# Performance work log

Hardware: AMD Instinct MI355X
Metric: run time of the kernel (lower is better)

The kernel has to match this reference:

```python
import jax, jax.numpy as jnp
import numpy as np

DIM = 1024
N_HEADS = 16
HEAD_DIM = DIM // N_HEADS
MAX_SEQ = 2048
BATCH = 4
SEQ = 2048


def _rope_tables(seq_len, head_dim):
    inv_freq = 1.0 / (10000.0 ** (jnp.arange(0, head_dim, 2, dtype=jnp.float32) / head_dim))
    t = jnp.arange(seq_len, dtype=jnp.float32)
    freqs = jnp.outer(t, inv_freq)            # [S, D/2]
    emb = jnp.concatenate([freqs, freqs], axis=-1)  # [S, D]
    return jnp.cos(emb), jnp.sin(emb)


def setup_inputs() -> dict:
    key = jax.random.key(0)
    kx, kq, kk, kv, ko = jax.random.split(key, 5)
    s = 1.0 / np.sqrt(DIM)
    x = jax.random.normal(kx, (BATCH, SEQ, DIM), dtype=jnp.float32)
    Wq = jax.random.normal(kq, (DIM, DIM), dtype=jnp.float32) * s
    Wk = jax.random.normal(kk, (DIM, DIM), dtype=jnp.float32) * s
    Wv = jax.random.normal(kv, (DIM, DIM), dtype=jnp.float32) * s
    Wo = jax.random.normal(ko, (DIM, DIM), dtype=jnp.float32) * s
    cos, sin = _rope_tables(SEQ, HEAD_DIM)
    mask = jnp.tril(jnp.ones((SEQ, SEQ), dtype=bool))[None, None]  # [1,1,S,S] causal
    return {"x": x, "Wq": Wq, "Wk": Wk, "Wv": Wv, "Wo": Wo,
            "cos": cos, "sin": sin, "mask": mask}


def _rotate_half(t):
    t1, t2 = jnp.split(t, 2, axis=-1)
    return jnp.concatenate([-t2, t1], axis=-1)


def reference(x, Wq, Wk, Wv, Wo, cos, sin, mask):
    B, S, _ = x.shape
    # projections (torch Linear: y = x @ W.T)
    q = (x @ Wq.T).reshape(B, S, N_HEADS, HEAD_DIM)
    k = (x @ Wk.T).reshape(B, S, N_HEADS, HEAD_DIM)
    v = (x @ Wv.T).reshape(B, S, N_HEADS, HEAD_DIM)
    # RoPE on [B,S,H,D]: cos/sin broadcast over batch and heads
    c = cos[None, :S, None, :]
    s_ = sin[None, :S, None, :]
    q = q * c + _rotate_half(q) * s_
    k = k * c + _rotate_half(k) * s_
    # attention, heads-major
    scale = HEAD_DIM ** -0.5
    attn = jnp.einsum('bqhd,bkhd->bhqk', q, k) * scale
    attn = jnp.where(mask, attn, -jnp.inf)
    attn = jax.nn.softmax(attn, axis=-1)
    out = jnp.einsum('bhqk,bkhd->bqhd', attn, v).reshape(B, S, DIM)
    return out @ Wo.T
```

## Files before the change

kernel.cpp:

```cpp
#include <hip/hip_runtime.h>
#include <hip/hip_bf16.h>
#include <stdint.h>

typedef __bf16 bf16;
typedef __bf16 bf16x4 __attribute__((ext_vector_type(4)));
typedef __bf16 bf16x8 __attribute__((ext_vector_type(8)));
typedef float f32x4 __attribute__((ext_vector_type(4)));

static constexpr int DIMM  = 1024;
static constexpr int NHEADS = 16;
static constexpr int HDIM  = 64;
static constexpr int SEQL  = 2048;
static constexpr int NB    = 4;
static constexpr int MTOT  = NB * SEQL;
static constexpr float LOG2E = 1.4426950408889634f;

__device__ __forceinline__ bool probe_fp32(const void* cosT) {
    return *(const uint32_t*)cosT != 0x3F803F80u;
}

__device__ __forceinline__ bf16x8 load8_any(const void* p, size_t off, bool f32) {
    if (f32) {
        const float* q = (const float*)p + off;
        f32x4 a = *(const f32x4*)q;
        f32x4 b = *(const f32x4*)(q + 4);
        bf16x8 r;
        r[0] = (bf16)a[0]; r[1] = (bf16)a[1]; r[2] = (bf16)a[2]; r[3] = (bf16)a[3];
        r[4] = (bf16)b[0]; r[5] = (bf16)b[1]; r[6] = (bf16)b[2]; r[7] = (bf16)b[3];
        return r;
    }
    return *(const bf16x8*)((const bf16*)p + off);
}

__device__ __forceinline__ float loadf_any(const void* p, size_t off, bool f32) {
    return f32 ? ((const float*)p)[off] : (float)((const bf16*)p)[off];
}

__device__ __forceinline__ int swz(int row, int kc) {
    return row * 128 + ((kc ^ (row & 7)) << 4);
}

__device__ __forceinline__ void gl_lds16(const bf16* g, bf16* l) {
    __builtin_amdgcn_global_load_lds(
        (const __attribute__((address_space(1))) unsigned int*)g,
        (__attribute__((address_space(3))) unsigned int*)l,
        16, 0, 0);
}

__global__ __launch_bounds__(256)
void cvt_kernel(const void* __restrict__ x,  const void* __restrict__ Wq,
                const void* __restrict__ Wk, const void* __restrict__ Wv,
                const void* __restrict__ Wo, const void* __restrict__ cosT,
                bf16* __restrict__ xb,  bf16* __restrict__ Wqb,
                bf16* __restrict__ Wkb, bf16* __restrict__ Wvb,
                bf16* __restrict__ Wob)
{
    const bool f32 = probe_fp32(cosT);
    const size_t NX = (size_t)MTOT * DIMM;
    const size_t NW = (size_t)DIMM * DIMM;
    size_t i = ((size_t)blockIdx.x * 256 + threadIdx.x) * 8;
    const void* src; bf16* dst; size_t off;
    if (i < NX) { src = x; dst = xb; off = i; }
    else {
        size_t j = i - NX;
        int wsel = (int)(j >> 20);
        off = j & (NW - 1);
        if      (wsel == 0) { src = Wq; dst = Wqb; }
        else if (wsel == 1) { src = Wk; dst = Wkb; }
        else if (wsel == 2) { src = Wv; dst = Wvb; }
        else                { src = Wo; dst = Wob; }
    }
    *(bf16x8*)(dst + off) = load8_any(src, off, f32);
}

template <class AAddr, class BAddr>
__device__ __forceinline__ void gemm_tile_gl(AAddr ga, BAddr gb,
                                             bf16* As, bf16* Bs, f32x4 acc[4][4])
{
    const int tid  = threadIdx.x;
    const int lane = tid & 63;
    const int w    = tid >> 6;
    const int l15  = lane & 15;
    const int lg   = lane >> 4;
    const int r8   = lane >> 3;
    const int c8   = lane & 7;
    const int wm   = (w >> 1) * 64;
    const int wn   = (w & 1) * 64;

    #pragma unroll
    for (int mf = 0; mf < 4; ++mf)
        #pragma unroll
        for (int nf = 0; nf < 4; ++nf)
            acc[mf][nf] = f32x4{0.f, 0.f, 0.f, 0.f};

    for (int kt = 0; kt < DIMM / 64; ++kt) {
        const int k0 = kt * 64;
        #pragma unroll
        for (int i = 0; i < 4; ++i) {
            const int c   = w * 4 + i;
            const int row = c * 8 + r8;
            gl_lds16(ga(row, k0 + c8 * 8), As + c * 512);
            gl_lds16(gb(row, k0 + c8 * 8), Bs + c * 512);
        }
        __syncthreads();
        #pragma unroll
        for (int ks = 0; ks < 2; ++ks) {
            bf16x8 af[4], bfr[4];
            #pragma unroll
            for (int mf = 0; mf < 4; ++mf)
                af[mf] = *(const bf16x8*)(As + (wm + mf * 16 + l15) * 64 + (ks * 4 + lg) * 8);
            #pragma unroll
            for (int nf = 0; nf < 4; ++nf)
                bfr[nf] = *(const bf16x8*)(Bs + (wn + nf * 16 + l15) * 64 + (ks * 4 + lg) * 8);
            #pragma unroll
            for (int mf = 0; mf < 4; ++mf)
                #pragma unroll
                for (int nf = 0; nf < 4; ++nf)
                    acc[mf][nf] = __builtin_amdgcn_mfma_f32_16x16x32_bf16(
                        af[mf], bfr[nf], acc[mf][nf], 0, 0, 0);
        }
        __syncthreads();
    }
}

__global__ __launch_bounds__(256, 2)
void qkv_kernel(const bf16* __restrict__ xb,
                const bf16* __restrict__ Wqb, const bf16* __restrict__ Wkb,
                const bf16* __restrict__ Wvb,
                const void* __restrict__ cosT, const void* __restrict__ sinT,
                bf16* __restrict__ qb, bf16* __restrict__ kb, bf16* __restrict__ vTb)
{
    __shared__ __align__(16) bf16 As[2][128 * 32];
    __shared__ __align__(16) bf16 Bq[2][128 * 32];
    __shared__ __align__(16) bf16 Bk[2][128 * 32];
    __shared__ __align__(16) bf16 Bv[2][128 * 32];

    const bool f32 = probe_fp32(cosT);
    const int bm = (int)blockIdx.x * 128;
    const int bn = (int)blockIdx.y * 128;

    const int tid  = threadIdx.x;
    const int lane = tid & 63;
    const int w    = tid >> 6;
    const int l15  = lane & 15;
    const int lg   = lane >> 4;
    const int wm   = (w >> 1) * 64;
    const int wn   = (w & 1) * 64;

    f32x4 acc[3][4][4];
    #pragma unroll
    for (int w3 = 0; w3 < 3; ++w3)
        #pragma unroll
        for (int mf = 0; mf < 4; ++mf)
            #pragma unroll
            for (int nf = 0; nf < 4; ++nf)
                acc[w3][mf][nf] = f32x4{0.f, 0.f, 0.f, 0.f};

    const int c0  = w * 2;
    const int rp0 = lane >> 3;
    const int tt  = (lane & 7) ^ rp0;
    const int rgo = (tt >> 2) << 6;
    const int kq  = (tt & 3) * 8;

    auto stage = [&](int t, int buf) {
        const int k0 = t * 32;
        #pragma unroll
        for (int i = 0; i < 2; ++i) {
            const int c  = c0 + i;
            const int rg = c * 8 + rp0 + rgo;
            const size_t am = (size_t)(bm + rg) * DIMM + k0 + kq;
            const size_t an = (size_t)(bn + rg) * DIMM + k0 + kq;
            gl_lds16(xb  + am, &As[buf][c * 512]);
            gl_lds16(Wqb + an, &Bq[buf][c * 512]);
            gl_lds16(Wkb + an, &Bk[buf][c * 512]);
            gl_lds16(Wvb + an, &Bv[buf][c * 512]);
        }
    };

    auto rd = [&](const bf16* base, int row) {
        return *(const bf16x8*)((const char*)base +
            (row & 63) * 128 + (((((row >> 6) << 2) | lg) ^ (row & 7)) << 4));
    };

    auto compute = [&](int buf) {
        bf16x8 af[4];
        #pragma unroll
        for (int mf = 0; mf < 4; ++mf)
            af[mf] = rd(As[buf], wm + mf * 16 + l15);
        const bf16* bsel[3] = {Bq[buf], Bk[buf], Bv[buf]};
        #pragma unroll
        for (int w3 = 0; w3 < 3; ++w3) {
            bf16x8 bfr[4];
            #pragma unroll
            for (int nf = 0; nf < 4; ++nf)
                bfr[nf] = rd(bsel[w3], wn + nf * 16 + l15);
            #pragma unroll
            for (int mf = 0; mf < 4; ++mf)
                #pragma unroll
                for (int nf = 0; nf < 4; ++nf)
                    acc[w3][mf][nf] = __builtin_amdgcn_mfma_f32_16x16x32_bf16(
                        af[mf], bfr[nf], acc[w3][mf][nf], 0, 0, 0);
        }
    };

    stage(0, 0);
    for (int t = 0; t < 31; ++t) {
        stage(t + 1, (t + 1) & 1);
        asm volatile("s_waitcnt vmcnt(8)" ::: "memory");
        __builtin_amdgcn_s_barrier();
        __builtin_amdgcn_sched_barrier(0);
        compute(t & 1);
        __builtin_amdgcn_sched_barrier(0);
        __builtin_amdgcn_s_barrier();
    }
    asm volatile("s_waitcnt vmcnt(0)" ::: "memory");
    __builtin_amdgcn_s_barrier();
    __builtin_amdgcn_sched_barrier(0);
    compute(1);

    #pragma unroll
    for (int mf = 0; mf < 4; ++mf) {
        #pragma unroll
        for (int nf = 0; nf < 4; ++nf) {
            int n = bn + wn + nf * 16 + l15;
            int h = n >> 6;
            int d = n & 63;
            float sign = (d < 32) ? -1.f : 1.f;
            #pragma unroll
            for (int r = 0; r < 4; ++r) {
                int m = bm + wm + mf * 16 + lg * 4 + r;
                int b = m >> 11, s = m & 2047;
                float c  = loadf_any(cosT, s * 64 + d, f32);
                float sv = loadf_any(sinT, s * 64 + d, f32);
                size_t o_qk = ((size_t)((b * NHEADS + h) * SEQL + s)) * HDIM + d;
                float q0 = acc[0][mf][nf][r], q1 = acc[0][mf][nf ^ 2][r];
                float k0v = acc[1][mf][nf][r], k1 = acc[1][mf][nf ^ 2][r];
                qb[o_qk] = (bf16)((q0 * c + sign * q1 * sv) * (0.125f * LOG2E));
                kb[o_qk] = (bf16)(k0v * c + sign * k1 * sv);
                vTb[((size_t)((b * NHEADS + h) * HDIM + d)) * SEQL + s] = (bf16)acc[2][mf][nf][r];
            }
        }
    }
}

__global__ __launch_bounds__(256, 3)
void attn_kernel(bf16* __restrict__ qb, const bf16* __restrict__ kb,
                 const bf16* __restrict__ vTb)
{
    __shared__ __align__(16) bf16 Ks[2][64 * 64];
    __shared__ __align__(16) bf16 Vs[2][64 * 64];
    __shared__ __align__(16) bf16 Pl[4][32 * 64];

    const int bh  = blockIdx.x;
    const int qt  = 15 - (int)blockIdx.y;
    const int tid = threadIdx.x;
    const int lane = tid & 63, w = tid >> 6;
    const int l15 = lane & 15, lg = lane >> 4;

    bf16*       Qp = qb  + (size_t)bh * SEQL * HDIM;
    const bf16* Kp = kb  + (size_t)bh * SEQL * HDIM;
    const bf16* Vp = vTb + (size_t)bh * HDIM * SEQL;

    const int q0  = qt * 128 + w * 32;
    const int njt = 2 * qt + 2;

    bf16x8 qf[2][2];
    #pragma unroll
    for (int mf = 0; mf < 2; ++mf)
        #pragma unroll
        for (int ks = 0; ks < 2; ++ks)
            qf[mf][ks] = *(const bf16x8*)(Qp + (size_t)(q0 + mf * 16 + l15) * HDIM + ks * 32 + lg * 8);

    f32x4 oacc[4][2];
    float lsum[2] = {0.f, 0.f};
    #pragma unroll
    for (int nd = 0; nd < 4; ++nd)
        #pragma unroll
        for (int mf = 0; mf < 2; ++mf)
            oacc[nd][mf] = f32x4{0.f, 0.f, 0.f, 0.f};

    char* Pw = (char*)Pl[w];
    const int l7 = l15 & 7;
    const int srow0 = tid >> 3;
    const int skc   = tid & 7;

    bf16x8 kr[2], vr[2];
    auto issue = [&](int j) {
        const int kk0 = j * 64;
        #pragma unroll
        for (int c = 0; c < 2; ++c) {
            int row = c * 32 + srow0;
            kr[c] = *(const bf16x8*)(Kp + (size_t)(kk0 + row) * HDIM + skc * 8);
            vr[c] = *(const bf16x8*)(Vp + (size_t)row * SEQL + kk0 + skc * 8);
        }
    };
    auto commit = [&](int b) {
        #pragma unroll
        for (int c = 0; c < 2; ++c) {
            int row = c * 32 + srow0;
            *(bf16x8*)((char*)Ks[b] + swz(row, skc)) = kr[c];
            *(bf16x8*)((char*)Vs[b] + swz(row, skc)) = vr[c];
        }
    };

    issue(0);
    commit(0);
    __syncthreads();

    for (int j = 0; j < njt; ++j) {
        const int kk0 = j * 64;
        const int buf = j & 1;
        const bool more = (j + 1 < njt);
        if (more) issue(j + 1);

        f32x4 sacc[4][2];
        #pragma unroll
        for (int nf = 0; nf < 4; ++nf)
            #pragma unroll
            for (int mf = 0; mf < 2; ++mf)
                sacc[nf][mf] = f32x4{0.f, 0.f, 0.f, 0.f};
        #pragma unroll
        for (int ks = 0; ks < 2; ++ks) {
            bf16x8 kf[4];
            #pragma unroll
            for (int nf = 0; nf < 4; ++nf)
                kf[nf] = *(const bf16x8*)((const char*)Ks[buf] + swz(nf * 16 + l15, ks * 4 + lg));
            #pragma unroll
            for (int nf = 0; nf < 4; ++nf)
                #pragma unroll
                for (int mf = 0; mf < 2; ++mf)
                    sacc[nf][mf] = __builtin_amdgcn_mfma_f32_16x16x32_bf16(
                        kf[nf], qf[mf][ks], sacc[nf][mf], 0, 0, 0);
        }

        const bool nm = (kk0 + 63 > q0);
        #pragma unroll
        for (int nf = 0; nf < 4; ++nf) {
            #pragma unroll
            for (int mf = 0; mf < 2; ++mf) {
                float pv[4];
                #pragma unroll
                for (int r = 0; r < 4; ++r) {
                    float s = sacc[nf][mf][r];
                    if (nm) {
                        int kv = kk0 + nf * 16 + lg * 4 + r;
                        int qq = q0 + mf * 16 + l15;
                        if (kv > qq) s = -1.0e30f;
                    }
                    pv[r] = exp2f(s);
                }
                lsum[mf] += (pv[0] + pv[1]) + (pv[2] + pv[3]);
                bf16x4 pb;
                pb[0] = (bf16)pv[0]; pb[1] = (bf16)pv[1];
                pb[2] = (bf16)pv[2]; pb[3] = (bf16)pv[3];
                *(bf16x4*)(Pw + (mf * 16 + l15) * 128
                              + (((2 * nf + (lg >> 1)) ^ l7) << 4) + (lg & 1) * 8) = pb;
            }
        }

        #pragma unroll
        for (int ks = 0; ks < 2; ++ks) {
            bf16x8 pf[2], vf[4];
            #pragma unroll
            for (int mf = 0; mf < 2; ++mf)
                pf[mf] = *(const bf16x8*)(Pw + (mf * 16 + l15) * 128
                                             + (((ks * 4 + lg) ^ l7) << 4));
            #pragma unroll
            for (int nd = 0; nd < 4; ++nd)
                vf[nd] = *(const bf16x8*)((const char*)Vs[buf] + swz(nd * 16 + l15, ks * 4 + lg));
            #pragma unroll
            for (int nd = 0; nd < 4; ++nd)
                #pragma unroll
                for (int mf = 0; mf < 2; ++mf)
                    oacc[nd][mf] = __builtin_amdgcn_mfma_f32_16x16x32_bf16(
                        vf[nd], pf[mf], oacc[nd][mf], 0, 0, 0);
        }

        if (more) {
            commit(buf ^ 1);
            __syncthreads();
        }
    }

    #pragma unroll
    for (int mf = 0; mf < 2; ++mf) {
        lsum[mf] += __shfl_xor(lsum[mf], 16);
        lsum[mf] += __shfl_xor(lsum[mf], 32);
    }
    float inv[2] = {1.f / lsum[0], 1.f / lsum[1]};
    #pragma unroll
    for (int nd = 0; nd < 4; ++nd)
        #pragma unroll
        for (int mf = 0; mf < 2; ++mf) {
            bf16x4 o4;
            #pragma unroll
            for (int r = 0; r < 4; ++r)
                o4[r] = (bf16)(oacc[nd][mf][r] * inv[mf]);
            int s = q0 + mf * 16 + l15;
            int d = nd * 16 + lg * 4;
            *(bf16x4*)(Qp + (size_t)s * HDIM + d) = o4;
        }
}

__global__ __launch_bounds__(256)
void oproj_kernel(const bf16* __restrict__ O, const bf16* __restrict__ Wob,
                  const void* __restrict__ cosT, void* __restrict__ outp)
{
    __shared__ __align__(16) bf16 As[128 * 64];
    __shared__ __align__(16) bf16 Bs[128 * 64];
    const bool f32 = probe_fp32(cosT);
    const int bm = blockIdx.x * 128;
    const int bn = blockIdx.y * 128;

    f32x4 acc[4][4];
    gemm_tile_gl(
        [&](int row, int k) {
            int m = bm + row;
            int b = m >> 11, s = m & 2047;
            int h = k >> 6, dd = k & 63;
            return O + ((size_t)((b * NHEADS + h) * SEQL + s)) * HDIM + dd;
        },
        [&](int row, int k) { return Wob + (size_t)(bn + row) * DIMM + k; },
        As, Bs, acc);

    const int tid = threadIdx.x;
    const int lane = tid & 63, wid = tid >> 6;
    const int l15 = lane & 15, lg = lane >> 4;
    const int wm = (wid >> 1) * 64, wn = (wid & 1) * 64;

    #pragma unroll
    for (int mf = 0; mf < 4; ++mf)
        #pragma unroll
        for (int nf = 0; nf < 4; ++nf) {
            int n = bn + wn + nf * 16 + l15;
            #pragma unroll
            for (int r = 0; r < 4; ++r) {
                int m = bm + wm + mf * 16 + lg * 4 + r;
                float v = acc[mf][nf][r];
                if (f32) ((float*)outp)[(size_t)m * DIMM + n] = v;
                else     ((bf16*)outp)[(size_t)m * DIMM + n] = (bf16)v;
            }
        }
}

extern "C" void kernel_launch(void* const* d_in, const int* in_sizes, int n_in,
                              void* d_out, int out_size, void* d_ws, size_t ws_size,
                              hipStream_t stream)
{
    const void* x    = d_in[0];
    const void* Wq   = d_in[1];
    const void* Wk   = d_in[2];
    const void* Wv   = d_in[3];
    const void* Wo   = d_in[4];
    const void* cosT = d_in[5];
    const void* sinT = d_in[6];

    const size_t NELEM = (size_t)MTOT * DIMM;
    const size_t NW    = (size_t)DIMM * DIMM;
    bf16* qb  = (bf16*)d_ws;
    bf16* kb  = qb + NELEM;
    bf16* vT  = kb + NELEM;
    bf16* xb  = vT + NELEM;
    bf16* Wqb = xb + NELEM;
    bf16* Wkb = Wqb + NW;
    bf16* Wvb = Wkb + NW;
    bf16* Wob = Wvb + NW;

    dim3 blk(256);
    cvt_kernel<<<dim3(6144), blk, 0, stream>>>(x, Wq, Wk, Wv, Wo, cosT,
                                               xb, Wqb, Wkb, Wvb, Wob);

    dim3 g1(MTOT / 128, DIMM / 128);
    qkv_kernel<<<g1, blk, 0, stream>>>(xb, Wqb, Wkb, Wvb, cosT, sinT, qb, kb, vT);

    dim3 g2(NB * NHEADS, SEQL / 128);
    attn_kernel<<<g2, blk, 0, stream>>>(qb, kb, vT);

    dim3 g3(MTOT / 128, DIMM / 128);
    oproj_kernel<<<g3, blk, 0, stream>>>(qb, Wob, cosT, d_out);
}
```

Baseline: 174.5 us.

## Fuse x fp32-to-bf16 conversion into QKV GEMM and register-stage A operands

Drops the separate conversion pass over x. The QKV kernel now loads fp32 x straight into registers, converts it to bf16 in the MFMA loop, and double-buffers these A fragments in registers instead of staging them through LDS. The output projection is also rewritten to load O fragments directly into registers and double-buffer only the weight tiles in LDS, with occupancy raised. The fp32/bf16 runtime probe is removed, so inputs are now assumed to be fp32, and each qkv block reloads x fp32 from global memory for every N tile, which doubles A-side read bytes.

```diff
diff --git a/kernel.cpp b/kernel.cpp
--- a/kernel.cpp
+++ b/kernel.cpp
@@ -15,27 +15,6 @@
 static constexpr int MTOT  = NB * SEQL;
 static constexpr float LOG2E = 1.4426950408889634f;
 
-__device__ __forceinline__ bool probe_fp32(const void* cosT) {
-    return *(const uint32_t*)cosT != 0x3F803F80u;
-}
-
-__device__ __forceinline__ bf16x8 load8_any(const void* p, size_t off, bool f32) {
-    if (f32) {
-        const float* q = (const float*)p + off;
-        f32x4 a = *(const f32x4*)q;
-        f32x4 b = *(const f32x4*)(q + 4);
-        bf16x8 r;
-        r[0] = (bf16)a[0]; r[1] = (bf16)a[1]; r[2] = (bf16)a[2]; r[3] = (bf16)a[3];
-        r[4] = (bf16)b[0]; r[5] = (bf16)b[1]; r[6] = (bf16)b[2]; r[7] = (bf16)b[3];
-        return r;
-    }
-    return *(const bf16x8*)((const bf16*)p + off);
-}
-
-__device__ __forceinline__ float loadf_any(const void* p, size_t off, bool f32) {
-    return f32 ? ((const float*)p)[off] : (float)((const bf16*)p)[off];
-}
-
 __device__ __forceinline__ int swz(int row, int kc) {
     return row * 128 + ((kc ^ (row & 7)) << 4);
 }
@@ -47,95 +26,44 @@
         16, 0, 0);
 }
 
+__device__ __forceinline__ bf16x8 cvt8(f32x4 a, f32x4 b) {
+    bf16x8 r;
+    r[0] = (bf16)a[0]; r[1] = (bf16)a[1]; r[2] = (bf16)a[2]; r[3] = (bf16)a[3];
+    r[4] = (bf16)b[0]; r[5] = (bf16)b[1]; r[6] = (bf16)b[2]; r[7] = (bf16)b[3];
+    return r;
+}
+
 __global__ __launch_bounds__(256)
-void cvt_kernel(const void* __restrict__ x,  const void* __restrict__ Wq,
-                const void* __restrict__ Wk, const void* __restrict__ Wv,
-                const void* __restrict__ Wo, const void* __restrict__ cosT,
-                bf16* __restrict__ xb,  bf16* __restrict__ Wqb,
-                bf16* __restrict__ Wkb, bf16* __restrict__ Wvb,
-                bf16* __restrict__ Wob)
+void cvt_kernel(const float* __restrict__ Wq, const float* __restrict__ Wk,
+                const float* __restrict__ Wv, const float* __restrict__ Wo,
+                bf16* __restrict__ Wqb, bf16* __restrict__ Wkb,
+                bf16* __restrict__ Wvb, bf16* __restrict__ Wob)
 {
-    const bool f32 = probe_fp32(cosT);
-    const size_t NX = (size_t)MTOT * DIMM;
     const size_t NW = (size_t)DIMM * DIMM;
     size_t i = ((size_t)blockIdx.x * 256 + threadIdx.x) * 8;
-    const void* src; bf16* dst; size_t off;
-    if (i < NX) { src = x; dst = xb; off = i; }
-    else {
-        size_t j = i - NX;
-        int wsel = (int)(j >> 20);
-        off = j & (NW - 1);
-        if      (wsel == 0) { src = Wq; dst = Wqb; }
-        else if (wsel == 1) { src = Wk; dst = Wkb; }
-        else if (wsel == 2) { src = Wv; dst = Wvb; }
-        else                { src = Wo; dst = Wob; }
-    }
-    *(bf16x8*)(dst + off) = load8_any(src, off, f32);
-}
-
-template <class AAddr, class BAddr>
-__device__ __forceinline__ void gemm_tile_gl(AAddr ga, BAddr gb,
-                                             bf16* As, bf16* Bs, f32x4 acc[4][4])
-{
-    const int tid  = threadIdx.x;
-    const int lane = tid & 63;
-    const int w    = tid >> 6;
-    const int l15  = lane & 15;
-    const int lg   = lane >> 4;
-    const int r8   = lane >> 3;
-    const int c8   = lane & 7;
-    const int wm   = (w >> 1) * 64;
-    const int wn   = (w & 1) * 64;
-
-    #pragma unroll
-    for (int mf = 0; mf < 4; ++mf)
-        #pragma unroll
-        for (int nf = 0; nf < 4; ++nf)
-            acc[mf][nf] = f32x4{0.f, 0.f, 0.f, 0.f};
-
-    for (int kt = 0; kt < DIMM / 64; ++kt) {
-        const int k0 = kt * 64;
-        #pragma unroll
-        for (int i = 0; i < 4; ++i) {
-            const int c   = w * 4 + i;
-            const int row = c * 8 + r8;
-            gl_lds16(ga(row, k0 + c8 * 8), As + c * 512);
-            gl_lds16(gb(row, k0 + c8 * 8), Bs + c * 512);
-        }
-        __syncthreads();
-        #pragma unroll
-        for (int ks = 0; ks < 2; ++ks) {
-            bf16x8 af[4], bfr[4];
-            #pragma unroll
-            for (int mf = 0; mf < 4; ++mf)
-                af[mf] = *(const bf16x8*)(As + (wm + mf * 16 + l15) * 64 + (ks * 4 + lg) * 8);
-            #pragma unroll
-            for (int nf = 0; nf < 4; ++nf)
-                bfr[nf] = *(const bf16x8*)(Bs + (wn + nf * 16 + l15) * 64 + (ks * 4 + lg) * 8);
-            #pragma unroll
-            for (int mf = 0; mf < 4; ++mf)
-                #pragma unroll
-                for (int nf = 0; nf < 4; ++nf)
-                    acc[mf][nf] = __builtin_amdgcn_mfma_f32_16x16x32_bf16(
-                        af[mf], bfr[nf], acc[mf][nf], 0, 0, 0);
-        }
-        __syncthreads();
-    }
+    int wsel = (int)(i >> 20);
+    size_t off = i & (NW - 1);
+    const float* src; bf16* dst;
+    if      (wsel == 0) { src = Wq; dst = Wqb; }
+    else if (wsel == 1) { src = Wk; dst = Wkb; }
+    else if (wsel == 2) { src = Wv; dst = Wvb; }
+    else                { src = Wo; dst = Wob; }
+    f32x4 a = *(const f32x4*)(src + off);
+    f32x4 b = *(const f32x4*)(src + off + 4);
+    *(bf16x8*)(dst + off) = cvt8(a, b);
 }
 
 __global__ __launch_bounds__(256, 2)
-void qkv_kernel(const bf16* __restrict__ xb,
+void qkv_kernel(const float* __restrict__ xf,
                 const bf16* __restrict__ Wqb, const bf16* __restrict__ Wkb,
                 const bf16* __restrict__ Wvb,
-                const void* __restrict__ cosT, const void* __restrict__ sinT,
+                const float* __restrict__ cosT, const float* __restrict__ sinT,
                 bf16* __restrict__ qb, bf16* __restrict__ kb, bf16* __restrict__ vTb)
 {
-    __shared__ __align__(16) bf16 As[2][128 * 32];
     __shared__ __align__(16) bf16 Bq[2][128 * 32];
     __shared__ __align__(16) bf16 Bk[2][128 * 32];
     __shared__ __align__(16) bf16 Bv[2][128 * 32];
 
-    const bool f32 = probe_fp32(cosT);
     const int bm = (int)blockIdx.x * 128;
     const int bn = (int)blockIdx.y * 128;
 
@@ -162,31 +90,39 @@
     const int rgo = (tt >> 2) << 6;
     const int kq  = (tt & 3) * 8;
 
-    auto stage = [&](int t, int buf) {
+    auto stageB = [&](int t, int buf) {
         const int k0 = t * 32;
         #pragma unroll
         for (int i = 0; i < 2; ++i) {
             const int c  = c0 + i;
             const int rg = c * 8 + rp0 + rgo;
-            const size_t am = (size_t)(bm + rg) * DIMM + k0 + kq;
             const size_t an = (size_t)(bn + rg) * DIMM + k0 + kq;
-            gl_lds16(xb  + am, &As[buf][c * 512]);
             gl_lds16(Wqb + an, &Bq[buf][c * 512]);
             gl_lds16(Wkb + an, &Bk[buf][c * 512]);
             gl_lds16(Wvb + an, &Bv[buf][c * 512]);
         }
     };
 
+    auto loadA = [&](f32x4 (&dst)[8], int t) {
+        const int k0 = t * 32;
+        #pragma unroll
+        for (int mf = 0; mf < 4; ++mf) {
+            const float* p = xf + (size_t)(bm + wm + mf * 16 + l15) * DIMM + k0 + lg * 8;
+            dst[2 * mf]     = *(const f32x4*)p;
+            dst[2 * mf + 1] = *(const f32x4*)(p + 4);
+        }
+    };
+
     auto rd = [&](const bf16* base, int row) {
         return *(const bf16x8*)((const char*)base +
             (row & 63) * 128 + (((((row >> 6) << 2) | lg) ^ (row & 7)) << 4));
     };
 
-    auto compute = [&](int buf) {
+    auto compute = [&](int buf, const f32x4 (&a)[8]) {
         bf16x8 af[4];
         #pragma unroll
         for (int mf = 0; mf < 4; ++mf)
-            af[mf] = rd(As[buf], wm + mf * 16 + l15);
+            af[mf] = cvt8(a[2 * mf], a[2 * mf + 1]);
         const bf16* bsel[3] = {Bq[buf], Bk[buf], Bv[buf]};
         #pragma unroll
         for (int w3 = 0; w3 < 3; ++w3) {
@@ -203,20 +139,35 @@
         }
     };
 
-    stage(0, 0);
-    for (int t = 0; t < 31; ++t) {
-        stage(t + 1, (t + 1) & 1);
-        asm volatile("s_waitcnt vmcnt(8)" ::: "memory");
+    f32x4 aA[8], aB[8];
+
+    stageB(0, 0);
+    __builtin_amdgcn_sched_barrier(0);
+    loadA(aA, 0);
+    __builtin_amdgcn_sched_barrier(0);
+
+    auto step = [&](f32x4 (&cur)[8], f32x4 (&nxt)[8], int t) {
+        stageB(t + 1, (t + 1) & 1);
+        __builtin_amdgcn_sched_barrier(0);
+        asm volatile("s_waitcnt vmcnt(14)" ::: "memory");
         __builtin_amdgcn_s_barrier();
         __builtin_amdgcn_sched_barrier(0);
-        compute(t & 1);
+        loadA(nxt, t + 1);
+        compute(t & 1, cur);
         __builtin_amdgcn_sched_barrier(0);
         __builtin_amdgcn_s_barrier();
+    };
+
+    #pragma unroll 1
+    for (int tp = 0; tp < 15; ++tp) {
+        step(aA, aB, 2 * tp);
+        step(aB, aA, 2 * tp + 1);
     }
+    step(aA, aB, 30);
     asm volatile("s_waitcnt vmcnt(0)" ::: "memory");
     __builtin_amdgcn_s_barrier();
     __builtin_amdgcn_sched_barrier(0);
-    compute(1);
+    compute(1, aB);
 
     #pragma unroll
     for (int mf = 0; mf < 4; ++mf) {
@@ -230,8 +181,8 @@
             for (int r = 0; r < 4; ++r) {
                 int m = bm + wm + mf * 16 + lg * 4 + r;
                 int b = m >> 11, s = m & 2047;
-                float c  = loadf_any(cosT, s * 64 + d, f32);
-                float sv = loadf_any(sinT, s * 64 + d, f32);
+                float c  = cosT[s * 64 + d];
+                float sv = sinT[s * 64 + d];
                 size_t o_qk = ((size_t)((b * NHEADS + h) * SEQL + s)) * HDIM + d;
                 float q0 = acc[0][mf][nf][r], q1 = acc[0][mf][nf ^ 2][r];
                 float k0v = acc[1][mf][nf][r], k1 = acc[1][mf][nf ^ 2][r];
@@ -402,31 +353,105 @@
         }
 }
 
-__global__ __launch_bounds__(256)
+__global__ __launch_bounds__(256, 2)
 void oproj_kernel(const bf16* __restrict__ O, const bf16* __restrict__ Wob,
-                  const void* __restrict__ cosT, void* __restrict__ outp)
+                  float* __restrict__ outp)
 {
-    __shared__ __align__(16) bf16 As[128 * 64];
-    __shared__ __align__(16) bf16 Bs[128 * 64];
-    const bool f32 = probe_fp32(cosT);
-    const int bm = blockIdx.x * 128;
-    const int bn = blockIdx.y * 128;
+    __shared__ __align__(16) bf16 Bs[2][128 * 32];
+
+    const int bm = (int)blockIdx.x * 128;
+    const int bn = (int)blockIdx.y * 128;
+
+    const int tid  = threadIdx.x;
+    const int lane = tid & 63;
+    const int w    = tid >> 6;
+    const int l15  = lane & 15;
+    const int lg   = lane >> 4;
+    const int wm   = (w >> 1) * 64;
+    const int wn   = (w & 1) * 64;
 
     f32x4 acc[4][4];
-    gemm_tile_gl(
-        [&](int row, int k) {
-            int m = bm + row;
+    #pragma unroll
+    for (int mf = 0; mf < 4; ++mf)
+        #pragma unroll
+        for (int nf = 0; nf < 4; ++nf)
+            acc[mf][nf] = f32x4{0.f, 0.f, 0.f, 0.f};
+
+    const int c0  = w * 2;
+    const int rp0 = lane >> 3;
+    const int tt  = (lane & 7) ^ rp0;
+    const int rgo = (tt >> 2) << 6;
+    const int kq  = (tt & 3) * 8;
+
+    auto stageB = [&](int t, int buf) {
+        const int k0 = t * 32;
+        #pragma unroll
+        for (int i = 0; i < 2; ++i) {
+            const int c  = c0 + i;
+            const int rg = c * 8 + rp0 + rgo;
+            gl_lds16(Wob + (size_t)(bn + rg) * DIMM + k0 + kq, &Bs[buf][c * 512]);
+        }
+    };
+
+    auto loadA = [&](bf16x8 (&dst)[4], int t) {
+        const int k0 = t * 32;
+        #pragma unroll
+        for (int mf = 0; mf < 4; ++mf) {
+            int m = bm + wm + mf * 16 + l15;
             int b = m >> 11, s = m & 2047;
+            int k = k0 + lg * 8;
             int h = k >> 6, dd = k & 63;
-            return O + ((size_t)((b * NHEADS + h) * SEQL + s)) * HDIM + dd;
-        },
-        [&](int row, int k) { return Wob + (size_t)(bn + row) * DIMM + k; },
-        As, Bs, acc);
-
-    const int tid = threadIdx.x;
-    const int lane = tid & 63, wid = tid >> 6;
-    const int l15 = lane & 15, lg = lane >> 4;
-    const int wm = (wid >> 1) * 64, wn = (wid & 1) * 64;
+            dst[mf] = *(const bf16x8*)(O + ((size_t)((b * NHEADS + h) * SEQL + s)) * HDIM + dd);
+        }
+    };
+
+    auto rd = [&](const bf16* base, int row) {
+        return *(const bf16x8*)((const char*)base +
+            (row & 63) * 128 + (((((row >> 6) << 2) | lg) ^ (row & 7)) << 4));
+    };
+
+    auto compute = [&](int buf, const bf16x8 (&af)[4]) {
+        bf16x8 bfr[4];
+        #pragma unroll
+        for (int nf = 0; nf < 4; ++nf)
+            bfr[nf] = rd(Bs[buf], wn + nf * 16 + l15);
+        #pragma unroll
+        for (int mf = 0; mf < 4; ++mf)
+            #pragma unroll
+            for (int nf = 0; nf < 4; ++nf)
+                acc[mf][nf] = __builtin_amdgcn_mfma_f32_16x16x32_bf16(
+                    af[mf], bfr[nf], acc[mf][nf], 0, 0, 0);
+    };
+
+    bf16x8 aA[4], aB[4];
+
+    stageB(0, 0);
+    __builtin_amdgcn_sched_barrier(0);
+    loadA(aA, 0);
+    __builtin_amdgcn_sched_barrier(0);
+
+    auto step = [&](bf16x8 (&cur)[4], bf16x8 (&nxt)[4], int t) {
+        stageB(t + 1, (t + 1) & 1);
+        __builtin_amdgcn_sched_barrier(0);
+        asm volatile("s_waitcnt vmcnt(6)" ::: "memory");
+        __builtin_amdgcn_s_barrier();
+        __builtin_amdgcn_sched_barrier(0);
+        loadA(nxt, t + 1);
+        compute(t & 1, cur);
+        __builtin_amdgcn_sched_barrier(0);
+        __builtin_amdgcn_s_barrier();
+    };
+
+    #pragma unroll 1
+    for (int tp = 0; tp < 15; ++tp) {
+        step(aA, aB, 2 * tp);
+        step(aB, aA, 2 * tp + 1);
+    }
+    step(aA, aB, 30);
+    asm volatile("s_waitcnt vmcnt(0)" ::: "memory");
+    __builtin_amdgcn_s_barrier();
+    __builtin_amdgcn_sched_barrier(0);
+    compute(1, aB);
 
     #pragma unroll
     for (int mf = 0; mf < 4; ++mf)
@@ -436,9 +461,7 @@
             #pragma unroll
             for (int r = 0; r < 4; ++r) {
                 int m = bm + wm + mf * 16 + lg * 4 + r;
-                float v = acc[mf][nf][r];
-                if (f32) ((float*)outp)[(size_t)m * DIMM + n] = v;
-                else     ((bf16*)outp)[(size_t)m * DIMM + n] = (bf16)v;
+                outp[(size_t)m * DIMM + n] = acc[mf][nf][r];
             }
         }
 }
@@ -447,35 +470,33 @@
                               void* d_out, int out_size, void* d_ws, size_t ws_size,
                               hipStream_t stream)
 {
-    const void* x    = d_in[0];
-    const void* Wq   = d_in[1];
-    const void* Wk   = d_in[2];
-    const void* Wv   = d_in[3];
-    const void* Wo   = d_in[4];
-    const void* cosT = d_in[5];
-    const void* sinT = d_in[6];
+    const float* x    = (const float*)d_in[0];
+    const float* Wq   = (const float*)d_in[1];
+    const float* Wk   = (const float*)d_in[2];
+    const float* Wv   = (const float*)d_in[3];
+    const float* Wo   = (const float*)d_in[4];
+    const float* cosT = (const float*)d_in[5];
+    const float* sinT = (const float*)d_in[6];
 
     const size_t NELEM = (size_t)MTOT * DIMM;
     const size_t NW    = (size_t)DIMM * DIMM;
     bf16* qb  = (bf16*)d_ws;
     bf16* kb  = qb + NELEM;
     bf16* vT  = kb + NELEM;
-    bf16* xb  = vT + NELEM;
-    bf16* Wqb = xb + NELEM;
+    bf16* Wqb = vT + NELEM;
     bf16* Wkb = Wqb + NW;
     bf16* Wvb = Wkb + NW;
     bf16* Wob = Wvb + NW;
 
     dim3 blk(256);
-    cvt_kernel<<<dim3(6144), blk, 0, stream>>>(x, Wq, Wk, Wv, Wo, cosT,
-                                               xb, Wqb, Wkb, Wvb, Wob);
+    cvt_kernel<<<dim3(2048), blk, 0, stream>>>(Wq, Wk, Wv, Wo, Wqb, Wkb, Wvb, Wob);
 
     dim3 g1(MTOT / 128, DIMM / 128);
-    qkv_kernel<<<g1, blk, 0, stream>>>(xb, Wqb, Wkb, Wvb, cosT, sinT, qb, kb, vT);
+    qkv_kernel<<<g1, blk, 0, stream>>>(x, Wqb, Wkb, Wvb, cosT, sinT, qb, kb, vT);
 
     dim3 g2(NB * NHEADS, SEQL / 128);
     attn_kernel<<<g2, blk, 0, stream>>>(qb, kb, vT);
 
     dim3 g3(MTOT / 128, DIMM / 128);
-    oproj_kernel<<<g3, blk, 0, stream>>>(qb, Wob, cosT, d_out);
-}
+    oproj_kernel<<<g3, blk, 0, stream>>>(qb, Wob, (float*)d_out);
+}
```

Result: slower. 298.0 us (+70.7%).
